# Kernel tuning notes

Measured on AMD Instinct MI355X. Metric: run time of the kernel, lower is better.

The kernel has to match this reference:

```python
import jax, jax.numpy as jnp
import numpy as np

N, E, DIN, H, C, L = 100000, 1600000, 128, 128, 40, 4
EPS = 1e-5  # BatchNorm1d default eps


def _bn(x, g, b):
    # training-mode batchnorm over node dim, biased variance (PyTorch normalizes
    # the batch with biased var in forward)
    m = jnp.mean(x, axis=0)
    v = jnp.var(x, axis=0)
    return g * (x - m) * jax.lax.rsqrt(v + EPS) + b


def _sage(h, src, dst, Wl_i, bl_i, Wr_i):
    # PyG SAGEConv (aggr='mean', root_weight=True): lin_l(mean_j x_j) + lin_r(x_i)
    msg = h[src]                                             # [E, H]
    s = jax.ops.segment_sum(msg, dst, num_segments=N)        # [N, H]
    cnt = jax.ops.segment_sum(jnp.ones((E, 1), h.dtype), dst, num_segments=N)
    agg = s / jnp.maximum(cnt, 1.0)
    return agg @ Wl_i + bl_i + h @ Wr_i


def setup_inputs() -> dict:
    key = jax.random.key(0)
    ks = jax.random.split(key, 14)
    s = 0.05
    x = jax.random.normal(ks[0], (N, DIN), dtype=jnp.float32)
    edge_index = jax.random.randint(ks[1], (2, E), 0, N)
    return {
        "x": x,
        "W_in": jax.random.normal(ks[2], (DIN, H), dtype=jnp.float32) * s,
        "b_in": jnp.zeros((H,), jnp.float32),
        "g_in": jnp.ones((H,), jnp.float32),
        "beta_in": jnp.zeros((H,), jnp.float32),
        "Wl": jax.random.normal(ks[3], (L, H, H), dtype=jnp.float32) * s,
        "bl": jnp.zeros((L, H), jnp.float32),
        "Wr": jax.random.normal(ks[4], (L, H, H), dtype=jnp.float32) * s,
        "g_bn": jnp.ones((L, H), jnp.float32),
        "b_bn": jnp.zeros((L, H), jnp.float32),
        "W_out": jax.random.normal(ks[5], (H, C), dtype=jnp.float32) * s,
        "b_out": jnp.zeros((C,), jnp.float32),
        "edge_index": edge_index,
    }


def reference(x, W_in, b_in, g_in, beta_in, Wl, bl, Wr, g_bn, b_bn, W_out, b_out, edge_index):
    src, dst = edge_index[0], edge_index[1]
    h = jax.nn.relu(_bn(x @ W_in + b_in, g_in, beta_in))  # dropout p=0.0 -> identity
    for i in range(L):
        h = _sage(h, src, dst, Wl[i], bl[i], Wr[i])
        if i < L - 1:
            h = jax.nn.relu(_bn(h, g_bn[i], b_bn[i]))
    return h @ W_out + b_out
```

## Files before the change

kernel.cpp:

```cpp
#include <hip/hip_runtime.h>

#define N_NODES 100000
#define N_EDGES 1600000
#define HD 128
#define NLAYERS 4
#define COUT 40
#define BN_EPS 1e-5f
#define NBUCK 782
#define BUCK_CAP 3072
constexpr int GB = (N_NODES + 127) / 128;

typedef _Float16 half8 __attribute__((ext_vector_type(8)));
typedef float floatx4 __attribute__((ext_vector_type(4)));

__global__ void prep_kernel(const float* __restrict__ W_in,
                            const float* __restrict__ Wl,
                            const float* __restrict__ Wr,
                            const float* __restrict__ W_out,
                            _Float16* __restrict__ Wt_in,
                            _Float16* __restrict__ Wt_cat,
                            _Float16* __restrict__ Wt_out)
{
    int tid = blockIdx.x * blockDim.x + threadIdx.x;
    int stride = gridDim.x * blockDim.x;
    for (int idx = tid; idx < 128 * 128; idx += stride) {
        int n = idx >> 7, k = idx & 127;
        Wt_in[idx] = (_Float16)W_in[k * 128 + n];
    }
    for (int idx = tid; idx < 4 * 128 * 256; idx += stride) {
        int i = idx >> 15;
        int r = idx & 32767;
        int n = r >> 8, k = r & 255;
        Wt_cat[idx] = (_Float16)((k < 128) ? Wl[i * 16384 + k * 128 + n]
                                           : Wr[i * 16384 + (k - 128) * 128 + n]);
    }
    for (int idx = tid; idx < 48 * 128; idx += stride) {
        int n = idx >> 7, k = idx & 127;
        Wt_out[idx] = (n < COUT) ? (_Float16)W_out[k * COUT + n] : (_Float16)0.f;
    }
}

__global__ __launch_bounds__(256) void bucket_hist_kernel(const int* __restrict__ edst,
                                                          int* __restrict__ bcnt) {
    __shared__ int h[NBUCK];
    for (int b = threadIdx.x; b < NBUCK; b += 256) h[b] = 0;
    __syncthreads();
    int tid = blockIdx.x * 256 + threadIdx.x;
    int stride = gridDim.x * 256;
    for (int e = tid; e < N_EDGES; e += stride)
        atomicAdd(&h[edst[e] >> 7], 1);
    __syncthreads();
    for (int b = threadIdx.x; b < NBUCK; b += 256)
        if (h[b]) atomicAdd(&bcnt[b], h[b]);
}

__global__ void bucket_scan_kernel(const int* __restrict__ bcnt,
                                   int* __restrict__ bbase, int* __restrict__ bcur) {
    int lane = threadIdx.x;
    int run = 0;
    for (int base = 0; base < NBUCK; base += 64) {
        int i = base + lane;
        int orig = (i < NBUCK) ? bcnt[i] : 0;
        int v = orig;
        #pragma unroll
        for (int off = 1; off < 64; off <<= 1) {
            int t = __shfl_up(v, off);
            if (lane >= off) v += t;
        }
        int total = __shfl(v, 63);
        int excl = v - orig + run;
        if (i < NBUCK) { bbase[i] = excl; bcur[i] = excl; }
        run += total;
    }
    if (lane == 0) bbase[NBUCK] = run;
}

#define SCAT_T 16
__global__ __launch_bounds__(512) void bucket_scatter_kernel(const int* __restrict__ esrc,
                                                             const int* __restrict__ edst,
                                                             int* __restrict__ bcur,
                                                             int* __restrict__ bedges) {
    __shared__ int cnt[NBUCK], gpos[NBUCK];
    long base = (long)blockIdx.x * (512 * SCAT_T);
    for (int b = threadIdx.x; b < NBUCK; b += 512) cnt[b] = 0;
    __syncthreads();
    int srcs[SCAT_T], locs[SCAT_T], rnk[SCAT_T], bks[SCAT_T];
    #pragma unroll
    for (int j = 0; j < SCAT_T; ++j) {
        long e = base + j * 512 + threadIdx.x;
        if (e < N_EDGES) {
            int d = edst[e];
            srcs[j] = esrc[e];
            bks[j] = d >> 7;
            locs[j] = d & 127;
            rnk[j] = atomicAdd(&cnt[bks[j]], 1);
        } else bks[j] = -1;
    }
    __syncthreads();
    for (int b = threadIdx.x; b < NBUCK; b += 512) {
        int c = cnt[b];
        gpos[b] = c ? atomicAdd(&bcur[b], c) : 0;
    }
    __syncthreads();
    #pragma unroll
    for (int j = 0; j < SCAT_T; ++j)
        if (bks[j] >= 0)
            bedges[gpos[bks[j]] + rnk[j]] = (locs[j] << 17) | srcs[j];
}

__global__ __launch_bounds__(256) void bucket_sort_kernel(const int* __restrict__ bedges,
                                                          const int* __restrict__ bbase,
                                                          int* __restrict__ rs,
                                                          int* __restrict__ ssrc) {
    __shared__ int lsrc[BUCK_CAP];
    __shared__ int h[128], hin[128], lcur[128];
    int b = blockIdx.x;
    int s = bbase[b];
    int n = bbase[b + 1] - s;
    if (n > BUCK_CAP) n = BUCK_CAP;
    if (threadIdx.x < 128) h[threadIdx.x] = 0;
    __syncthreads();
    for (int i = threadIdx.x; i < n; i += 256) {
        int v = bedges[s + i];
        lsrc[i] = v;
        atomicAdd(&h[v >> 17], 1);
    }
    __syncthreads();
    if (threadIdx.x < 128) hin[threadIdx.x] = h[threadIdx.x];
    __syncthreads();
    #pragma unroll
    for (int off = 1; off < 128; off <<= 1) {
        int t = 0;
        if (threadIdx.x < 128 && (int)threadIdx.x >= off) t = h[threadIdx.x - off];
        __syncthreads();
        if (threadIdx.x < 128) h[threadIdx.x] += t;
        __syncthreads();
    }
    if (threadIdx.x < 128) {
        int excl = h[threadIdx.x] - hin[threadIdx.x];
        lcur[threadIdx.x] = excl;
        int node = b * 128 + threadIdx.x;
        if (node < N_NODES) rs[node] = s + excl;
    }
    if (b == NBUCK - 1 && threadIdx.x == 0) rs[N_NODES] = bbase[NBUCK];
    __syncthreads();
    for (int i = threadIdx.x; i < n; i += 256) {
        int v = lsrc[i];
        int r = atomicAdd(&lcur[v >> 17], 1);
        ssrc[s + r] = v & 0x1FFFF;
    }
}

__global__ __launch_bounds__(256) void aggregate_kernel(const _Float16* __restrict__ H,
                                                        const int* __restrict__ rs,
                                                        const int* __restrict__ ssrc,
                                                        _Float16* __restrict__ AGG) {
    int wid = (blockIdx.x * 256 + threadIdx.x) >> 6;
    int lane = threadIdx.x & 63;
    int grp = lane >> 4, l16 = lane & 15;
    int e0 = rs[wid], e1 = rs[wid + 1];
    int deg = e1 - e0;
    int q = (deg + 3) >> 2;
    int e = e0 + grp * q;
    int ge = min(e + q, e1);

    float acc[8] = {0.f, 0.f, 0.f, 0.f, 0.f, 0.f, 0.f, 0.f};
    const _Float16* __restrict__ Hc = H + l16 * 8;

    for (; e + 4 <= ge; e += 4) {
        int s0 = ssrc[e], s1 = ssrc[e + 1], s2 = ssrc[e + 2], s3 = ssrc[e + 3];
        half8 v0 = *(const half8*)(Hc + (long)s0 * HD);
        half8 v1 = *(const half8*)(Hc + (long)s1 * HD);
        half8 v2 = *(const half8*)(Hc + (long)s2 * HD);
        half8 v3 = *(const half8*)(Hc + (long)s3 * HD);
        #pragma unroll
        for (int j = 0; j < 8; ++j)
            acc[j] += ((float)v0[j] + (float)v1[j]) + ((float)v2[j] + (float)v3[j]);
    }
    for (; e < ge; ++e) {
        int s0 = ssrc[e];
        half8 v0 = *(const half8*)(Hc + (long)s0 * HD);
        #pragma unroll
        for (int j = 0; j < 8; ++j) acc[j] += (float)v0[j];
    }

    #pragma unroll
    for (int j = 0; j < 8; ++j) {
        acc[j] += __shfl_xor(acc[j], 16);
        acc[j] += __shfl_xor(acc[j], 32);
    }
    if (grp == 0) {
        float inv = 1.f / (float)max(deg, 1);
        half8 o;
        #pragma unroll
        for (int j = 0; j < 8; ++j) o[j] = (_Float16)(acc[j] * inv);
        *(half8*)(AGG + (long)wid * HD + l16 * 8) = o;
    }
}

template <int CT, int KS, bool HAS_A1, bool A_F32, bool OUT_F32, bool STATS>
__global__ __launch_bounds__(256, 2) void gemm_kernel(const void* __restrict__ A0v,
                                                      const _Float16* __restrict__ A1,
                                                      const _Float16* __restrict__ Wt,
                                                      const float* __restrict__ bias,
                                                      void* __restrict__ Yv,
                                                      int out_stride, int ncols,
                                                      float* __restrict__ gstats) {
    constexpr int K = KS * 32;
    constexpr int KSC = (KS > 4) ? 4 : KS;
    __shared__ _Float16 bsm[KSC * 32 * CT * 16];
    int wave = threadIdx.x >> 6;
    int lane = threadIdx.x & 63;
    int quad = lane >> 4;
    int l16 = lane & 15;
    int row_base = (blockIdx.x * 4 + wave) * 32;
    bool active = row_base < N_NODES;

    floatx4 acc[2][CT];
    #pragma unroll
    for (int rt = 0; rt < 2; ++rt)
        #pragma unroll
        for (int c = 0; c < CT; ++c)
            acc[rt][c] = (floatx4){0.f, 0.f, 0.f, 0.f};

    for (int ch = 0; ch < KS; ch += KSC) {
        if (ch) __syncthreads();
        for (int i = threadIdx.x; i < KSC * CT * 64; i += 256) {
            int n = i % (CT * 16);
            int ko = i / (CT * 16);
            half8 v = *(const half8*)(Wt + n * K + (ch * 4 + ko) * 8);
            int slot = (((ko >> 2) * CT + (n >> 4)) * 4 + (ko & 3)) * 16 + (n & 15);
            *(half8*)(bsm + slot * 8) = v;
        }
        __syncthreads();
        if (active) {
            #pragma unroll
            for (int s2 = 0; s2 < KSC; ++s2) {
                int s = ch + s2;
                int kk = s * 32 + quad * 8;
                half8 afrag[2];
                #pragma unroll
                for (int rt = 0; rt < 2; ++rt) {
                    int r = row_base + rt * 16 + l16;
                    if (r > N_NODES - 1) r = N_NODES - 1;
                    if (A_F32) {
                        const float* p = (const float*)A0v + (long)r * 128 + kk;
                        floatx4 f0 = *(const floatx4*)p;
                        floatx4 f1 = *(const floatx4*)(p + 4);
                        #pragma unroll
                        for (int j = 0; j < 4; ++j) {
                            afrag[rt][j]     = (_Float16)f0[j];
                            afrag[rt][4 + j] = (_Float16)f1[j];
                        }
                    } else {
                        const _Float16* p;
                        if (HAS_A1 && kk >= 128) p = A1 + (long)r * 128 + (kk - 128);
                        else                     p = (const _Float16*)A0v + (long)r * 128 + kk;
                        afrag[rt] = *(const half8*)p;
                    }
                }
                #pragma unroll
                for (int c = 0; c < CT; ++c) {
                    half8 bfrag = *(const half8*)(bsm + ((s2 * CT + c) * 64 + lane) * 8);
                    #pragma unroll
                    for (int rt = 0; rt < 2; ++rt)
                        acc[rt][c] = __builtin_amdgcn_mfma_f32_16x16x32_f16(afrag[rt], bfrag, acc[rt][c], 0, 0, 0);
                }
            }
        }
    }

    float* lsum = (float*)bsm;
    float* lsq  = lsum + 128;
    if (STATS) {
        __syncthreads();
        if (threadIdx.x < 128) { lsum[threadIdx.x] = 0.f; lsq[threadIdx.x] = 0.f; }
        __syncthreads();
    } else {
        if (!active) return;
    }

    #pragma unroll
    for (int c = 0; c < CT; ++c) {
        int col = c * 16 + l16;
        float s_c = 0.f, q_c = 0.f;
        if (active && col < ncols) {
            float bv = bias[col];
            #pragma unroll
            for (int rt = 0; rt < 2; ++rt) {
                #pragma unroll
                for (int i = 0; i < 4; ++i) {
                    int r = row_base + rt * 16 + quad * 4 + i;
                    if (r < N_NODES) {
                        float v = acc[rt][c][i] + bv;
                        if (OUT_F32) ((float*)Yv)[(long)r * out_stride + col] = v;
                        else         ((_Float16*)Yv)[(long)r * out_stride + col] = (_Float16)v;
                        if (STATS) { s_c += v; q_c += v * v; }
                    }
                }
            }
        }
        if (STATS) {
            s_c += __shfl_xor(s_c, 16); s_c += __shfl_xor(s_c, 32);
            q_c += __shfl_xor(q_c, 16); q_c += __shfl_xor(q_c, 32);
            if (lane < 16 && active) {
                atomicAdd(&lsum[col], s_c);
                atomicAdd(&lsq[col], q_c);
            }
        }
    }

    if (STATS) {
        __syncthreads();
        if (threadIdx.x < 128) {
            atomicAdd(&gstats[threadIdx.x], lsum[threadIdx.x]);
            atomicAdd(&gstats[128 + threadIdx.x], lsq[threadIdx.x]);
        }
    }
}

__global__ __launch_bounds__(256) void bn_apply_kernel(const _Float16* __restrict__ Y,
                                                       const float* __restrict__ gstats,
                                                       const float* __restrict__ g,
                                                       const float* __restrict__ b,
                                                       _Float16* __restrict__ H) {
    __shared__ float sc[128], sh[128];
    if (threadIdx.x < 128) {
        int col = threadIdx.x;
        float m = gstats[col] * (1.f / (float)N_NODES);
        float v = gstats[128 + col] * (1.f / (float)N_NODES) - m * m;
        float s = g[col] * rsqrtf(v + BN_EPS);
        sc[col] = s;
        sh[col] = b[col] - m * s;
    }
    __syncthreads();
    long total = (long)N_NODES * HD / 8;
    for (long t = (long)blockIdx.x * blockDim.x + threadIdx.x; t < total;
         t += (long)gridDim.x * blockDim.x) {
        long base = t * 8;
        int col0 = (int)(base & 127);
        half8 in = *(const half8*)(Y + base);
        half8 outv;
        #pragma unroll
        for (int j = 0; j < 8; ++j) {
            float v = (float)in[j];
            float r = v * sc[col0 + j] + sh[col0 + j];
            outv[j] = (_Float16)fmaxf(r, 0.f);
        }
        *(half8*)(H + base) = outv;
    }
}

extern "C" void kernel_launch(void* const* d_in, const int* in_sizes, int n_in,
                              void* d_out, int out_size, void* d_ws, size_t ws_size,
                              hipStream_t stream) {
    (void)in_sizes; (void)n_in; (void)out_size; (void)ws_size;
    const float* x       = (const float*)d_in[0];
    const float* W_in    = (const float*)d_in[1];
    const float* b_in    = (const float*)d_in[2];
    const float* g_in    = (const float*)d_in[3];
    const float* beta_in = (const float*)d_in[4];
    const float* Wl      = (const float*)d_in[5];
    const float* bl      = (const float*)d_in[6];
    const float* Wr      = (const float*)d_in[7];
    const float* g_bn    = (const float*)d_in[8];
    const float* b_bn    = (const float*)d_in[9];
    const float* W_out   = (const float*)d_in[10];
    const float* b_out   = (const float*)d_in[11];
    const int*   ei      = (const int*)d_in[12];
    const int* esrc = ei;
    const int* edst = ei + N_EDGES;
    float* out = (float*)d_out;

    char* w = (char*)d_ws;
    auto alloc = [&](size_t bytes) -> char* {
        char* p = w; w += (bytes + 255) & ~(size_t)255; return p;
    };
    int* rs           = (int*)alloc((N_NODES + 1) * sizeof(int));
    int* bcnt         = (int*)alloc((NBUCK + 1) * sizeof(int));
    int* bbase        = (int*)alloc((NBUCK + 1) * sizeof(int));
    int* bcur         = (int*)alloc(NBUCK * sizeof(int));
    int* ssrc         = (int*)alloc(N_EDGES * sizeof(int));
    _Float16* Wt_in   = (_Float16*)alloc(128 * 128 * 2);
    _Float16* Wt_cat  = (_Float16*)alloc(4 * 128 * 256 * 2);
    _Float16* Wt_out  = (_Float16*)alloc(48 * 128 * 2);
    _Float16* hbuf    = (_Float16*)alloc((size_t)N_NODES * HD * 2);
    _Float16* agg     = (_Float16*)alloc((size_t)N_NODES * HD * 2);
    _Float16* ybuf    = (_Float16*)alloc((size_t)N_NODES * HD * 2);
    float* gstats     = (float*)alloc(4 * 256 * 4);
    int* bedges       = (int*)agg;

    hipMemsetAsync(bcnt, 0, (NBUCK + 1) * sizeof(int), stream);
    hipMemsetAsync(gstats, 0, 4 * 256 * 4, stream);
    prep_kernel<<<256, 256, 0, stream>>>(W_in, Wl, Wr, W_out, Wt_in, Wt_cat, Wt_out);
    bucket_hist_kernel<<<64, 256, 0, stream>>>(edst, bcnt);
    bucket_scan_kernel<<<1, 64, 0, stream>>>(bcnt, bbase, bcur);
    bucket_scatter_kernel<<<(N_EDGES + 8191) / 8192, 512, 0, stream>>>(esrc, edst, bcur, bedges);
    bucket_sort_kernel<<<NBUCK, 256, 0, stream>>>(bedges, bbase, rs, ssrc);

    gemm_kernel<8, 4, false, true, false, true><<<GB, 256, 0, stream>>>(
        x, nullptr, Wt_in, b_in, ybuf, HD, HD, gstats);
    bn_apply_kernel<<<1600, 256, 0, stream>>>(ybuf, gstats, g_in, beta_in, hbuf);

    for (int i = 0; i < NLAYERS; ++i) {
        aggregate_kernel<<<N_NODES / 4, 256, 0, stream>>>(hbuf, rs, ssrc, agg);
        if (i < NLAYERS - 1) {
            float* gs = gstats + (i + 1) * 256;
            gemm_kernel<8, 8, true, false, false, true><<<GB, 256, 0, stream>>>(
                agg, hbuf, Wt_cat + i * 128 * 256, bl + i * 128, ybuf, HD, HD, gs);
            bn_apply_kernel<<<1600, 256, 0, stream>>>(ybuf, gs, g_bn + i * 128, b_bn + i * 128, hbuf);
        } else {
            gemm_kernel<8, 8, true, false, false, false><<<GB, 256, 0, stream>>>(
                agg, hbuf, Wt_cat + i * 128 * 256, bl + i * 128, ybuf, HD, HD, nullptr);
        }
    }

    gemm_kernel<3, 4, false, false, true, false><<<GB, 256, 0, stream>>>(
        ybuf, nullptr, Wt_out, b_out, out, COUT, COUT, nullptr);
}
```

Baseline: 661.2 us.

## Map one 16-lane group per destination node and accumulate in fp16

The aggregate kernel now gives each 16-lane group of a wave its own destination node instead of splitting one node's edges across four groups. This removes the cross-group shuffle reduction and launches a quarter as many blocks. Neighbor sums are now accumulated in packed fp16 vectors instead of fp32, which cuts conversion work. The cost is lower precision and possible load imbalance between the four nodes sharing a wave.

```diff
diff --git a/kernel.cpp b/kernel.cpp
--- a/kernel.cpp
+++ b/kernel.cpp
@@ -158,44 +158,32 @@
     int wid = (blockIdx.x * 256 + threadIdx.x) >> 6;
     int lane = threadIdx.x & 63;
     int grp = lane >> 4, l16 = lane & 15;
-    int e0 = rs[wid], e1 = rs[wid + 1];
+    int dst = wid * 4 + grp;
+    int e0 = rs[dst], e1 = rs[dst + 1];
     int deg = e1 - e0;
-    int q = (deg + 3) >> 2;
-    int e = e0 + grp * q;
-    int ge = min(e + q, e1);
-
-    float acc[8] = {0.f, 0.f, 0.f, 0.f, 0.f, 0.f, 0.f, 0.f};
+
+    half8 acca = {0, 0, 0, 0, 0, 0, 0, 0};
+    half8 accb = {0, 0, 0, 0, 0, 0, 0, 0};
     const _Float16* __restrict__ Hc = H + l16 * 8;
 
-    for (; e + 4 <= ge; e += 4) {
+    int e = e0;
+    for (; e + 4 <= e1; e += 4) {
         int s0 = ssrc[e], s1 = ssrc[e + 1], s2 = ssrc[e + 2], s3 = ssrc[e + 3];
         half8 v0 = *(const half8*)(Hc + (long)s0 * HD);
         half8 v1 = *(const half8*)(Hc + (long)s1 * HD);
         half8 v2 = *(const half8*)(Hc + (long)s2 * HD);
         half8 v3 = *(const half8*)(Hc + (long)s3 * HD);
-        #pragma unroll
-        for (int j = 0; j < 8; ++j)
-            acc[j] += ((float)v0[j] + (float)v1[j]) + ((float)v2[j] + (float)v3[j]);
-    }
-    for (; e < ge; ++e) {
-        int s0 = ssrc[e];
-        half8 v0 = *(const half8*)(Hc + (long)s0 * HD);
-        #pragma unroll
-        for (int j = 0; j < 8; ++j) acc[j] += (float)v0[j];
-    }
-
-    #pragma unroll
-    for (int j = 0; j < 8; ++j) {
-        acc[j] += __shfl_xor(acc[j], 16);
-        acc[j] += __shfl_xor(acc[j], 32);
-    }
-    if (grp == 0) {
-        float inv = 1.f / (float)max(deg, 1);
-        half8 o;
-        #pragma unroll
-        for (int j = 0; j < 8; ++j) o[j] = (_Float16)(acc[j] * inv);
-        *(half8*)(AGG + (long)wid * HD + l16 * 8) = o;
-    }
+        acca += v0 + v1;
+        accb += v2 + v3;
+    }
+    for (; e < e1; ++e) {
+        half8 v0 = *(const half8*)(Hc + (long)ssrc[e] * HD);
+        acca += v0;
+    }
+    half8 acc = acca + accb;
+    _Float16 inv = (_Float16)(1.f / (float)max(deg, 1));
+    acc *= inv;
+    *(half8*)(AGG + (long)dst * HD + l16 * 8) = acc;
 }
 
 template <int CT, int KS, bool HAS_A1, bool A_F32, bool OUT_F32, bool STATS>
@@ -403,7 +391,7 @@
     bn_apply_kernel<<<1600, 256, 0, stream>>>(ybuf, gstats, g_in, beta_in, hbuf);
 
     for (int i = 0; i < NLAYERS; ++i) {
-        aggregate_kernel<<<N_NODES / 4, 256, 0, stream>>>(hbuf, rs, ssrc, agg);
+        aggregate_kernel<<<N_NODES / 16, 256, 0, stream>>>(hbuf, rs, ssrc, agg);
         if (i < NLAYERS - 1) {
             float* gs = gstats + (i + 1) * 256;
             gemm_kernel<8, 8, true, false, false, true><<<GB, 256, 0, stream>>>(
```

After: 651.0 us. No clear change (-1.5%).
